# Kernel tuning notes

Measured on AMD Instinct MI355X. Metric: run time of the kernel, lower is better.

Reference implementation:

```python
import jax, jax.numpy as jnp
import numpy as np

B_, S_, F_ = 2, 1024, 1024          # batch, seq_len, in_features
H_, D_, R_ = 8, 64, 2               # num_heads, head_dim, rank
EPS_NORM = 1e-6
EPS_RMS = 1e-6


def setup_inputs() -> dict:
    key = jax.random.key(0)
    ks = jax.random.split(key, 9)
    inputs = jax.random.normal(ks[0], (B_, S_, F_), dtype=jnp.float32)
    mask = jax.random.bernoulli(ks[1], 0.05, (B_, S_))  # episode-reset mask
    carry = jax.random.normal(ks[2], (B_, H_, D_, D_), dtype=jnp.float32) * 0.05
    lecun = 1.0 / np.sqrt(F_)
    Wq = jax.random.normal(ks[3], (F_, H_ * D_), dtype=jnp.float32) * lecun
    Wk = jax.random.normal(ks[4], (F_, H_ * R_ * D_), dtype=jnp.float32) * lecun
    Wv = jax.random.normal(ks[5], (F_, H_ * R_ * D_), dtype=jnp.float32) * lecun
    Wb = jax.random.normal(ks[6], (F_, H_ * R_), dtype=jnp.float32) * lecun
    rms_scale = jnp.ones((H_ * D_,), dtype=jnp.float32)
    Wo = jax.random.normal(ks[7], (H_ * D_, F_), dtype=jnp.float32) * (1.0 / np.sqrt(H_ * D_))
    bo = jnp.zeros((F_,), dtype=jnp.float32)
    return dict(inputs=inputs, mask=mask, carry=carry, Wq=Wq, Wk=Wk, Wv=Wv,
                Wb=Wb, rms_scale=rms_scale, Wo=Wo, bo=bo)


def reference(inputs, mask, carry, Wq, Wk, Wv, Wb, rms_scale, Wo, bo):
    B, S, F = inputs.shape
    H, D, R = H_, D_, R_

    q = jax.nn.silu(inputs @ Wq).reshape(B, S, H, D)
    k = jax.nn.silu((inputs @ Wk).reshape(B, S, H, R, D))
    v = (inputs @ Wv).reshape(B, S, H, R, D)
    beta = jax.nn.sigmoid((inputs @ Wb).reshape(B, S, H, R))

    q = q / (jnp.linalg.norm(q, axis=-1, keepdims=True) + EPS_NORM)
    k = k / (jnp.linalg.norm(k, axis=-1, keepdims=True) + EPS_NORM)

    # Rank-R Householder-style per-timestep transition: loop over small fixed rank
    A = jnp.broadcast_to(jnp.eye(D, dtype=inputs.dtype), (B, S, H, D, D))
    Bst = jnp.zeros((B, S, H, D, D), dtype=inputs.dtype)
    for r in range(R):
        kr = k[:, :, :, r]          # [B,S,H,D]
        vr = v[:, :, :, r]          # [B,S,H,D]
        br = beta[:, :, :, r]       # [B,S,H]
        Ak = jnp.einsum('bshij,bshj->bshi', A, kr)
        A = A - jnp.einsum('bshi,bsh,bshj->bshij', Ak, br, kr)
        Bk = jnp.einsum('bshij,bshj->bshi', Bst, kr)
        Bst = Bst + jnp.einsum('bshi,bsh,bshj->bshij', vr - Bk, br, kr)

    # zero the transition where mask=1 (state reset)
    A = A * (1.0 - mask.astype(A.dtype))[:, :, None, None, None]

    def binary_operator(lhs, rhs):
        a_i, b_i = lhs
        a_j, b_j = rhs
        return jnp.matmul(a_i, a_j), jnp.matmul(b_i, a_j) + b_j

    A, Bst = jax.lax.associative_scan(binary_operator, (A, Bst), axis=1)

    carry_seq = jnp.matmul(carry[:, None], A) + Bst        # [B,S,H,D,D]
    x = jnp.einsum('bshij,bshj->bshi', carry_seq, q).reshape(B, S, H * D)
    x = x * jax.lax.rsqrt(jnp.mean(x * x, axis=-1, keepdims=True) + EPS_RMS) * rms_scale
    y = x @ Wo + bo
    return carry_seq[:, -1], y
```

## Files before the change

### kernel.cpp

```cpp
#include <hip/hip_runtime.h>
#include <hip/hip_bf16.h>

#define B_ 2
#define S_ 1024
#define F_ 1024
#define H_ 8
#define D_ 64
#define R_ 2
#define BH (B_*H_)
#define NC 16
#define CL (S_/NC)

#define QOFF 0
#define KOFF 512
#define VOFF 1536
#define BOFF 2560
#define NPROJ 2624

typedef __bf16 bf16x8 __attribute__((ext_vector_type(8)));
typedef unsigned short ushort8 __attribute__((ext_vector_type(8)));
typedef float f32x4 __attribute__((ext_vector_type(4)));

__device__ __forceinline__ unsigned short f2bf(float f) {
    unsigned u = __builtin_bit_cast(unsigned, f);
    unsigned r = u + 0x7FFFu + ((u >> 16) & 1u);
    return (unsigned short)(r >> 16);
}

__device__ __forceinline__ void gload_lds16(const void* g, void* l) {
    __builtin_amdgcn_global_load_lds(
        (const __attribute__((address_space(1))) void*)g,
        (__attribute__((address_space(3))) void*)l, 16, 0, 0);
}

template<int CTRL>
__device__ __forceinline__ float dppf(float x) {
    return __builtin_bit_cast(float, __builtin_amdgcn_update_dpp(
        0, __builtin_bit_cast(int, x), CTRL, 0xF, 0xF, true));
}
__device__ __forceinline__ float qsum8(float x) {
    x += dppf<0xB1>(x);
    x += dppf<0x4E>(x);
    x += dppf<0x141>(x);
    return x;
}

__global__ void k_mask_prep(const void* __restrict__ mraw, float* __restrict__ maskf, int n) {
    __shared__ int fmt;
    int t = threadIdx.x;
    if (t == 0) fmt = 0;
    __syncthreads();
    const unsigned int* u32 = (const unsigned int*)mraw;
    for (int g = t; g < n / 4; g += blockDim.x) {
        unsigned int v = u32[g];
        if (v == 0x3F800000u) atomicMax(&fmt, 2);
        else if (v != 0u && v != 1u) atomicMax(&fmt, 1);
    }
    __syncthreads();
    int f = fmt;
    const unsigned char* u8 = (const unsigned char*)mraw;
    const float* f32 = (const float*)mraw;
    for (int i = t; i < n; i += blockDim.x) {
        float mv;
        if (f == 1)      mv = u8[i] ? 1.f : 0.f;
        else if (f == 2) mv = (f32[i] != 0.f) ? 1.f : 0.f;
        else             mv = (u32[i] != 0u) ? 1.f : 0.f;
        maskf[i] = mv;
    }
}

__global__ void k_f32_to_bf16(const float* __restrict__ s, unsigned short* __restrict__ d, int n) {
    int i = (blockIdx.x * blockDim.x + threadIdx.x) * 4;
    if (i < n) {
        float4 v = *(const float4*)&s[i];
        d[i + 0] = f2bf(v.x); d[i + 1] = f2bf(v.y);
        d[i + 2] = f2bf(v.z); d[i + 3] = f2bf(v.w);
    }
}

__global__ __launch_bounds__(256) void k_transpose_to_bf16(
    const float* __restrict__ src, unsigned short* __restrict__ dst, int K, int N)
{
    __shared__ float tile[32][33];
    int bx = blockIdx.x, by = blockIdx.y;
    int tx = threadIdx.x & 31, ty = threadIdx.x >> 5;
#pragma unroll
    for (int i = 0; i < 32; i += 8)
        tile[ty + i][tx] = src[(size_t)(by * 32 + ty + i) * N + bx * 32 + tx];
    __syncthreads();
#pragma unroll
    for (int i = 0; i < 32; i += 8)
        dst[(size_t)(bx * 32 + ty + i) * K + by * 32 + tx] = f2bf(tile[tx][ty + i]);
}

__global__ void k_wb_pad(const float* __restrict__ Wb, unsigned short* __restrict__ dst) {
    int row = blockIdx.x;
    int c0 = threadIdx.x * 4;
#pragma unroll
    for (int c = c0; c < c0 + 4; ++c)
        dst[(size_t)row * 1024 + c] = (row < 16) ? f2bf(Wb[(size_t)c * 16 + row]) : (unsigned short)0;
}

__global__ __launch_bounds__(256) void k_gemm_bf16(
    const unsigned short* __restrict__ A, const unsigned short* __restrict__ Bt,
    const float* __restrict__ bias, float* __restrict__ C,
    int M, int N, int K)
{
    constexpr int BM = 128, BN = 64, BK = 64;
    __shared__ unsigned short sA[BM * BK];
    __shared__ unsigned short sB[BN * BK];
    int t = threadIdx.x;
    int w = t >> 6, l = t & 63;
    int rowb = blockIdx.y * BM, colb = blockIdx.x * BN;
    int wr = w >> 1, wc = w & 1;
    int fr = l & 15, kgrp = l >> 4;

    f32x4 acc[4][2];
#pragma unroll
    for (int m = 0; m < 4; ++m)
#pragma unroll
        for (int n = 0; n < 2; ++n) acc[m][n] = (f32x4){0.f, 0.f, 0.f, 0.f};

    int lrow_off = l >> 3;
    int kg_phys = l & 7;

    for (int k0 = 0; k0 < K; k0 += BK) {
        __syncthreads();
#pragma unroll
        for (int is = 0; is < 4; ++is) {
            int r0 = (w * 4 + is) * 8;
            int row = r0 + lrow_off;
            int kg_log = kg_phys ^ (row & 7);
            gload_lds16(A + (size_t)(rowb + row) * K + k0 + kg_log * 8, &sA[r0 * BK]);
        }
#pragma unroll
        for (int is = 0; is < 2; ++is) {
            int r0 = (w * 2 + is) * 8;
            int row = r0 + lrow_off;
            int kg_log = kg_phys ^ (row & 7);
            gload_lds16(Bt + (size_t)(colb + row) * K + k0 + kg_log * 8, &sB[r0 * BK]);
        }
        asm volatile("s_waitcnt vmcnt(0)" ::: "memory");
        __syncthreads();

#pragma unroll
        for (int kk = 0; kk < BK; kk += 32) {
            int kg = (kk >> 3) + kgrp;
            bf16x8 af[4], bfv[2];
#pragma unroll
            for (int m = 0; m < 4; ++m) {
                int row = wr * 64 + m * 16 + fr;
                ushort8 raw = *(const ushort8*)&sA[row * BK + (kg ^ (row & 7)) * 8];
                af[m] = __builtin_bit_cast(bf16x8, raw);
            }
#pragma unroll
            for (int n = 0; n < 2; ++n) {
                int row = wc * 32 + n * 16 + fr;
                ushort8 raw = *(const ushort8*)&sB[row * BK + (kg ^ (row & 7)) * 8];
                bfv[n] = __builtin_bit_cast(bf16x8, raw);
            }
#pragma unroll
            for (int m = 0; m < 4; ++m)
#pragma unroll
                for (int n = 0; n < 2; ++n)
                    acc[m][n] = __builtin_amdgcn_mfma_f32_16x16x32_bf16(af[m], bfv[n], acc[m][n], 0, 0, 0);
        }
    }

#pragma unroll
    for (int m = 0; m < 4; ++m)
#pragma unroll
        for (int n = 0; n < 2; ++n) {
            int grow0 = rowb + wr * 64 + m * 16 + kgrp * 4;
            int gcol  = colb + wc * 32 + n * 16 + fr;
            float bv = bias ? bias[gcol] : 0.f;
#pragma unroll
            for (int r = 0; r < 4; ++r)
                C[(size_t)(grow0 + r) * N + gcol] = acc[m][n][r] + bv;
        }
}

__global__ void k_silu_norm(float* __restrict__ buf, int ngroups,
                            int gshift, int gmask, int rowstride, int coloff) {
    int w = threadIdx.x >> 6;
    int l = threadIdx.x & 63;
    int g = blockIdx.x * 4 + w;
    if (g >= ngroups) return;
    size_t idx = (size_t)(g >> gshift) * rowstride + coloff + ((g & gmask) << 6) + l;
    float x = buf[idx];
    float s = x / (1.f + expf(-x));
    float ss = s * s;
#pragma unroll
    for (int m = 1; m < 64; m <<= 1) ss += __shfl_xor(ss, m);
    float nrm = sqrtf(ss) + 1e-6f;
    buf[idx] = s / nrm;
}

__global__ __launch_bounds__(1024) void k_chunk_transfer(
    const float* __restrict__ proj, const float* __restrict__ maskf,
    float* __restrict__ Ac, float* __restrict__ Bc, float* __restrict__ ab)
{
    int c = blockIdx.x;
    int bh = blockIdx.y;
    int b = bh >> 3, h = bh & 7;
    int t = threadIdx.x;
    int half = t >> 9;
    int tt = t & 511;
    int i = tt >> 3;
    int sub = tt & 7;
    int e0 = sub * 8;
    __shared__ float sK[CL][128];
    __shared__ float sQ[CL][64];
    __shared__ float4 sScal[CL];
    __shared__ float4 sDots[CL];

    size_t tokbase = (size_t)(b * S_ + c * CL);
#pragma unroll
    for (int it = 0; it < (CL * 32) / 1024; ++it) {
        int f = it * 1024 + t;
        int tok = f >> 5, wi = f & 31;
        *(float4*)&sK[tok][wi * 4] = *(const float4*)&proj[(tokbase + tok) * NPROJ + KOFF + h * 128 + wi * 4];
    }
    {
        int f = t;
        int tok = f >> 4, wi = f & 15;
        *(float4*)&sQ[tok][wi * 4] = *(const float4*)&proj[(tokbase + tok) * NPROJ + QOFF + h * 64 + wi * 4];
    }
    if (t < CL) {
        float r0 = proj[(tokbase + t) * NPROJ + BOFF + h * 2 + 0];
        float r1 = proj[(tokbase + t) * NPROJ + BOFF + h * 2 + 1];
        float ms = 1.f - maskf[tokbase + t];
        sScal[t] = make_float4(1.f / (1.f + expf(-r0)), 1.f / (1.f + expf(-r1)), ms, 0.f);
    }
    __syncthreads();

    if (t < 512) {
        int tok = t >> 3, s8 = (t & 7) * 8;
        float p01 = 0.f, p0q = 0.f, p1q = 0.f;
#pragma unroll
        for (int e = 0; e < 8; ++e) {
            float k0e = sK[tok][s8 + e];
            float k1e = sK[tok][64 + s8 + e];
            float qe  = sQ[tok][s8 + e];
            p01 = fmaf(k0e, k1e, p01);
            p0q = fmaf(k0e, qe,  p0q);
            p1q = fmaf(k1e, qe,  p1q);
        }
        p01 = qsum8(p01); p0q = qsum8(p0q); p1q = qsum8(p1q);
        if ((t & 7) == 0) sDots[tok] = make_float4(p01, p0q, p1q, 0.f);
    }
    __syncthreads();

    float St[8];
#pragma unroll
    for (int j = 0; j < 8; ++j)
        St[j] = (half == 0 && e0 + j == i) ? 1.f : 0.f;

    const float* vbase = &proj[tokbase * NPROJ + VOFF + h * 128];
    float v0 = 0.f, v1 = 0.f;
    if (half) { v0 = vbase[i]; v1 = vbase[64 + i]; }

    float* abdst = ab + ((size_t)bh * NC + c) * (size_t)(CL * 128) + half * 64 + i;

    for (int sl = 0; sl < CL; ++sl) {
        float vc0 = v0, vc1 = v1;
        if (half && sl + 1 < CL) {
            const float* nb = vbase + (size_t)(sl + 1) * NPROJ;
            v0 = nb[i]; v1 = nb[64 + i];
        }
        float4 sc = sScal[sl];
        float4 dt = sDots[sl];
        if (sc.z == 0.f) {
#pragma unroll
            for (int j = 0; j < 8; ++j) St[j] = 0.f;
        }
        float k0[8], k1[8], qq[8];
        *(float4*)&k0[0] = *(const float4*)&sK[sl][e0];
        *(float4*)&k0[4] = *(const float4*)&sK[sl][e0 + 4];
        *(float4*)&k1[0] = *(const float4*)&sK[sl][64 + e0];
        *(float4*)&k1[4] = *(const float4*)&sK[sl][64 + e0 + 4];
        *(float4*)&qq[0] = *(const float4*)&sQ[sl][e0];
        *(float4*)&qq[4] = *(const float4*)&sQ[sl][e0 + 4];
        float a0 = 0.f, a1 = 0.f, b0 = 0.f, b1 = 0.f, c0v = 0.f, c1v = 0.f;
#pragma unroll
        for (int q = 0; q < 4; ++q) {
            a0 = fmaf(St[q],     k0[q],     a0);
            a1 = fmaf(St[4 + q], k0[4 + q], a1);
            b0 = fmaf(St[q],     k1[q],     b0);
            b1 = fmaf(St[4 + q], k1[4 + q], b1);
            c0v = fmaf(St[q],     qq[q],     c0v);
            c1v = fmaf(St[4 + q], qq[4 + q], c1v);
        }
        float d0 = qsum8(a0 + a1);
        float d1 = qsum8(b0 + b1);
        float dq = qsum8(c0v + c1v);
        float c0, c1;
        if (half == 0) {
            c0 = -sc.x * d0;
            float u1 = fmaf(c0, dt.x, d1);
            c1 = -sc.y * u1;
        } else {
            c0 = sc.x * (vc0 - d0);
            float u1 = fmaf(c0, dt.x, d1);
            c1 = sc.y * (vc1 - u1);
        }
        float xv = fmaf(c1, dt.z, fmaf(c0, dt.y, dq));
        if (sub == 0) abdst[sl * 128] = xv;
#pragma unroll
        for (int j = 0; j < 8; ++j) {
            St[j] = fmaf(c0, k0[j], St[j]);
            St[j] = fmaf(c1, k1[j], St[j]);
        }
    }
    float* dst = (half == 0 ? Ac : Bc) + ((size_t)bh * NC + c) * 4096 + (size_t)i * 64 + e0;
    *(float4*)&dst[0] = make_float4(St[0], St[1], St[2], St[3]);
    *(float4*)&dst[4] = make_float4(St[4], St[5], St[6], St[7]);
}

__global__ __launch_bounds__(256) void k_combine(
    const float* __restrict__ Ac, const float* __restrict__ Bc,
    const float* __restrict__ carry, float* __restrict__ S0,
    float* __restrict__ carry_out)
{
    constexpr int SP = 68;
    int blk = blockIdx.x;
    int bh = blk >> 2, rg = blk & 3;
    int t = threadIdx.x;
    int i = t >> 4;
    int j0 = (t & 15) * 4;
    int gi = rg * 16 + i;
    __shared__ float sA[2][64 * 64];
    __shared__ float sS[16 * SP];

    size_t cb0 = (size_t)bh * NC * 4096;
#pragma unroll
    for (int s = 0; s < 4; ++s)
        gload_lds16(Ac + cb0 + (size_t)(s * 256 + t) * 4, &sA[0][(size_t)(s * 256 + (t & 192)) * 4]);
    float4 rB = *(const float4*)&Bc[cb0 + (size_t)gi * 64 + j0];
    float4 racc = *(const float4*)&carry[(size_t)bh * 4096 + (size_t)gi * 64 + j0];
    *(float4*)&sS[i * SP + j0] = racc;
    asm volatile("s_waitcnt vmcnt(0)" ::: "memory");
    __syncthreads();

    for (int c = 0; c < NC; ++c) {
        int cur = c & 1;
        size_t cb = cb0 + (size_t)c * 4096;
        float4 rBn;
        if (c + 1 < NC) {
#pragma unroll
            for (int s = 0; s < 4; ++s)
                gload_lds16(Ac + cb + 4096 + (size_t)(s * 256 + t) * 4,
                            &sA[cur ^ 1][(size_t)(s * 256 + (t & 192)) * 4]);
            rBn = *(const float4*)&Bc[cb + 4096 + (size_t)gi * 64 + j0];
        }
        *(float4*)&S0[cb + (size_t)gi * 64 + j0] = racc;
        float4 acc = rB;
        float4 ac2 = make_float4(0.f, 0.f, 0.f, 0.f);
#pragma unroll
        for (int p4 = 0; p4 < 16; p4 += 2) {
            float4 s0v = *(const float4*)&sS[i * SP + p4 * 4];
            float4 s1v = *(const float4*)&sS[i * SP + p4 * 4 + 4];
            float4 a0 = *(const float4*)&sA[cur][(p4 * 4 + 0) * 64 + j0];
            float4 a1 = *(const float4*)&sA[cur][(p4 * 4 + 1) * 64 + j0];
            float4 a2 = *(const float4*)&sA[cur][(p4 * 4 + 2) * 64 + j0];
            float4 a3 = *(const float4*)&sA[cur][(p4 * 4 + 3) * 64 + j0];
            float4 a4 = *(const float4*)&sA[cur][(p4 * 4 + 4) * 64 + j0];
            float4 a5 = *(const float4*)&sA[cur][(p4 * 4 + 5) * 64 + j0];
            float4 a6 = *(const float4*)&sA[cur][(p4 * 4 + 6) * 64 + j0];
            float4 a7 = *(const float4*)&sA[cur][(p4 * 4 + 7) * 64 + j0];
            acc.x = fmaf(s0v.x, a0.x, acc.x); acc.y = fmaf(s0v.x, a0.y, acc.y);
            acc.z = fmaf(s0v.x, a0.z, acc.z); acc.w = fmaf(s0v.x, a0.w, acc.w);
            ac2.x = fmaf(s0v.y, a1.x, ac2.x); ac2.y = fmaf(s0v.y, a1.y, ac2.y);
            ac2.z = fmaf(s0v.y, a1.z, ac2.z); ac2.w = fmaf(s0v.y, a1.w, ac2.w);
            acc.x = fmaf(s0v.z, a2.x, acc.x); acc.y = fmaf(s0v.z, a2.y, acc.y);
            acc.z = fmaf(s0v.z, a2.z, acc.z); acc.w = fmaf(s0v.z, a2.w, acc.w);
            ac2.x = fmaf(s0v.w, a3.x, ac2.x); ac2.y = fmaf(s0v.w, a3.y, ac2.y);
            ac2.z = fmaf(s0v.w, a3.z, ac2.z); ac2.w = fmaf(s0v.w, a3.w, ac2.w);
            acc.x = fmaf(s1v.x, a4.x, acc.x); acc.y = fmaf(s1v.x, a4.y, acc.y);
            acc.z = fmaf(s1v.x, a4.z, acc.z); acc.w = fmaf(s1v.x, a4.w, acc.w);
            ac2.x = fmaf(s1v.y, a5.x, ac2.x); ac2.y = fmaf(s1v.y, a5.y, ac2.y);
            ac2.z = fmaf(s1v.y, a5.z, ac2.z); ac2.w = fmaf(s1v.y, a5.w, ac2.w);
            acc.x = fmaf(s1v.z, a6.x, acc.x); acc.y = fmaf(s1v.z, a6.y, acc.y);
            acc.z = fmaf(s1v.z, a6.z, acc.z); acc.w = fmaf(s1v.z, a6.w, acc.w);
            ac2.x = fmaf(s1v.w, a7.x, ac2.x); ac2.y = fmaf(s1v.w, a7.y, ac2.y);
            ac2.z = fmaf(s1v.w, a7.z, ac2.z); ac2.w = fmaf(s1v.w, a7.w, ac2.w);
        }
        acc.x += ac2.x; acc.y += ac2.y; acc.z += ac2.z; acc.w += ac2.w;
        __syncthreads();
        *(float4*)&sS[i * SP + j0] = acc;
        racc = acc;
        rB = rBn;
        asm volatile("s_waitcnt vmcnt(0)" ::: "memory");
        __syncthreads();
    }
    *(float4*)&carry_out[(size_t)bh * 4096 + (size_t)gi * 64 + j0] = racc;
}

__global__ __launch_bounds__(256) void k_xgemm(
    const float* __restrict__ ab, const float* __restrict__ S0,
    float* __restrict__ proj)
{
    constexpr int P = 67;
    int c = blockIdx.x, bh = blockIdx.y;
    int b = bh >> 3, h = bh & 7;
    int t = threadIdx.x;
    __shared__ float sAaT[64 * P];
    __shared__ float sS0T[64 * P];
    size_t abbase = ((size_t)bh * NC + c) * (size_t)(CL * 128);
    size_t s0base = ((size_t)bh * NC + c) * 4096;

#pragma unroll
    for (int it = 0; it < 4; ++it) {
        int f = it * 256 + t;
        int r = f >> 4, p0 = (f & 15) * 4;
        float4 va = *(const float4*)&ab[abbase + (size_t)r * 128 + p0];
        sAaT[(p0 + 0) * P + r] = va.x; sAaT[(p0 + 1) * P + r] = va.y;
        sAaT[(p0 + 2) * P + r] = va.z; sAaT[(p0 + 3) * P + r] = va.w;
        float4 vs = *(const float4*)&S0[s0base + (size_t)r * 64 + p0];
        sS0T[(p0 + 0) * P + r] = vs.x; sS0T[(p0 + 1) * P + r] = vs.y;
        sS0T[(p0 + 2) * P + r] = vs.z; sS0T[(p0 + 3) * P + r] = vs.w;
    }
    __syncthreads();

    int s0r = (t >> 4) * 4;
    int i0 = (t & 15) * 4;
    size_t tokbase = (size_t)(b * S_ + c * CL);
    float4 acc[4];
#pragma unroll
    for (int a = 0; a < 4; ++a)
        acc[a] = *(const float4*)&ab[abbase + (size_t)(s0r + a) * 128 + 64 + i0];
#pragma unroll 8
    for (int p = 0; p < 64; ++p) {
        float4 aa = *(const float4*)&sAaT[p * P + s0r];
        float4 ss = *(const float4*)&sS0T[p * P + i0];
        acc[0].x = fmaf(aa.x, ss.x, acc[0].x); acc[0].y = fmaf(aa.x, ss.y, acc[0].y);
        acc[0].z = fmaf(aa.x, ss.z, acc[0].z); acc[0].w = fmaf(aa.x, ss.w, acc[0].w);
        acc[1].x = fmaf(aa.y, ss.x, acc[1].x); acc[1].y = fmaf(aa.y, ss.y, acc[1].y);
        acc[1].z = fmaf(aa.y, ss.z, acc[1].z); acc[1].w = fmaf(aa.y, ss.w, acc[1].w);
        acc[2].x = fmaf(aa.z, ss.x, acc[2].x); acc[2].y = fmaf(aa.z, ss.y, acc[2].y);
        acc[2].z = fmaf(aa.z, ss.z, acc[2].z); acc[2].w = fmaf(aa.z, ss.w, acc[2].w);
        acc[3].x = fmaf(aa.w, ss.x, acc[3].x); acc[3].y = fmaf(aa.w, ss.y, acc[3].y);
        acc[3].z = fmaf(aa.w, ss.z, acc[3].z); acc[3].w = fmaf(aa.w, ss.w, acc[3].w);
    }
#pragma unroll
    for (int a = 0; a < 4; ++a)
        *(float4*)&proj[(tokbase + s0r + a) * NPROJ + QOFF + h * 64 + i0] = acc[a];
}

__global__ void k_rms_bf16(const float* __restrict__ proj, const float* __restrict__ scale,
                           unsigned short* __restrict__ xo) {
    int w = threadIdx.x >> 6;
    int l = threadIdx.x & 63;
    size_t row = (size_t)blockIdx.x * 4 + w;
    float4 v0 = *(const float4*)&proj[row * NPROJ + l * 8];
    float4 v1 = *(const float4*)&proj[row * NPROJ + l * 8 + 4];
    float ss = v0.x * v0.x + v0.y * v0.y + v0.z * v0.z + v0.w * v0.w
             + v1.x * v1.x + v1.y * v1.y + v1.z * v1.z + v1.w * v1.w;
#pragma unroll
    for (int m = 1; m < 64; m <<= 1) ss += __shfl_xor(ss, m);
    float sc = rsqrtf(ss * (1.f / 512.f) + 1e-6f);
    float4 s0 = *(const float4*)&scale[l * 8];
    float4 s1 = *(const float4*)&scale[l * 8 + 4];
    ushort8 o;
    o[0] = f2bf(v0.x * sc * s0.x); o[1] = f2bf(v0.y * sc * s0.y);
    o[2] = f2bf(v0.z * sc * s0.z); o[3] = f2bf(v0.w * sc * s0.w);
    o[4] = f2bf(v1.x * sc * s1.x); o[5] = f2bf(v1.y * sc * s1.y);
    o[6] = f2bf(v1.z * sc * s1.z); o[7] = f2bf(v1.w * sc * s1.w);
    *(ushort8*)&xo[row * 512 + l * 8] = o;
}

extern "C" void kernel_launch(void* const* d_in, const int* in_sizes, int n_in,
                              void* d_out, int out_size, void* d_ws, size_t ws_size,
                              hipStream_t stream) {
    const float* inputs    = (const float*)d_in[0];
    const void*  mask      = d_in[1];
    const float* carry     = (const float*)d_in[2];
    const float* Wq        = (const float*)d_in[3];
    const float* Wk        = (const float*)d_in[4];
    const float* Wv        = (const float*)d_in[5];
    const float* Wb        = (const float*)d_in[6];
    const float* rms_scale = (const float*)d_in[7];
    const float* Wo        = (const float*)d_in[8];
    const float* bo        = (const float*)d_in[9];

    float* out_carry = (float*)d_out;
    float* out_y     = (float*)d_out + (size_t)B_ * H_ * D_ * D_;

    const int M = B_ * S_;
    float* ws = (float*)d_ws;
    size_t o = 0;
    float* proj = ws + o; o += (size_t)M * NPROJ;
    float* mf   = ws + o; o += (size_t)M;
    float* Ac   = ws + o; o += (size_t)BH * NC * 4096;
    float* Bc   = ws + o; o += (size_t)BH * NC * 4096;
    float* S0   = ws + o; o += (size_t)BH * NC * 4096;
    float* abuf = ws + o; o += (size_t)BH * NC * CL * 128;
    unsigned short* wt = (unsigned short*)(ws + o); o += (size_t)NPROJ * 512;
    unsigned short* inb = (unsigned short*)Bc;
    unsigned short* xbf = (unsigned short*)Ac;

    k_mask_prep<<<1, 256, 0, stream>>>(mask, mf, M);
    k_f32_to_bf16<<<(M * 1024) / 1024, 256, 0, stream>>>(inputs, inb, M * 1024);

    k_transpose_to_bf16<<<dim3(512 / 32, 1024 / 32), 256, 0, stream>>>(Wq, wt + (size_t)QOFF * 1024, 1024, 512);
    k_transpose_to_bf16<<<dim3(1024 / 32, 1024 / 32), 256, 0, stream>>>(Wk, wt + (size_t)KOFF * 1024, 1024, 1024);
    k_transpose_to_bf16<<<dim3(1024 / 32, 1024 / 32), 256, 0, stream>>>(Wv, wt + (size_t)VOFF * 1024, 1024, 1024);
    k_wb_pad<<<64, 256, 0, stream>>>(Wb, wt + (size_t)BOFF * 1024);

    k_gemm_bf16<<<dim3(NPROJ / 64, M / 128), 256, 0, stream>>>(inb, wt, nullptr, proj, M, NPROJ, 1024);

    k_silu_norm<<<(M * 8) / 4, 256, 0, stream>>>(proj, M * 8, 3, 7, NPROJ, QOFF);
    k_silu_norm<<<(M * 16) / 4, 256, 0, stream>>>(proj, M * 16, 4, 15, NPROJ, KOFF);

    k_chunk_transfer<<<dim3(NC, BH), 1024, 0, stream>>>(proj, mf, Ac, Bc, abuf);
    k_combine<<<BH * 4, 256, 0, stream>>>(Ac, Bc, carry, S0, out_carry);
    k_xgemm<<<dim3(NC, BH), 256, 0, stream>>>(abuf, S0, proj);

    k_rms_bf16<<<M / 4, 256, 0, stream>>>(proj, rms_scale, xbf);

    k_transpose_to_bf16<<<dim3(1024 / 32, 512 / 32), 256, 0, stream>>>(Wo, wt, 512, 1024);
    k_gemm_bf16<<<dim3(1024 / 64, M / 128), 256, 0, stream>>>(xbf, wt, bo, out_y, M, 1024, 512);
}
```

Measured before the change: 138.5 us.

## Split scan into 32 short chunks with pairwise merge and fixup

The sequential per-chunk transfer kernel now processes 32 chunks of 32 tokens instead of 16 chunks of 64. This halves the serial loop length per block and doubles the block count. Adjacent chunk pairs are merged into 16 transitions for the existing inter-chunk combine. A new fixup kernel then recovers the start state of each even sub-chunk from the combined state. The change adds two small 64x64 matmul kernel launches and extra workspace traffic in exchange for a shorter serial critical path in the chunk scan.

```diff
diff --git a/kernel.cpp b/kernel.cpp
--- a/kernel.cpp
+++ b/kernel.cpp
@@ -9,7 +9,8 @@
 #define R_ 2
 #define BH (B_*H_)
 #define NC 16
-#define CL (S_/NC)
+#define NCT 32
+#define CT (S_/NCT)
 
 #define QOFF 0
 #define KOFF 512
@@ -209,24 +210,21 @@
     int i = tt >> 3;
     int sub = tt & 7;
     int e0 = sub * 8;
-    __shared__ float sK[CL][128];
-    __shared__ float sQ[CL][64];
-    __shared__ float4 sScal[CL];
-    __shared__ float4 sDots[CL];
-
-    size_t tokbase = (size_t)(b * S_ + c * CL);
-#pragma unroll
-    for (int it = 0; it < (CL * 32) / 1024; ++it) {
-        int f = it * 1024 + t;
-        int tok = f >> 5, wi = f & 31;
+    __shared__ float sK[CT][128];
+    __shared__ float sQ[CT][64];
+    __shared__ float4 sScal[CT];
+    __shared__ float4 sDots[CT];
+
+    size_t tokbase = (size_t)(b * S_ + c * CT);
+    {
+        int tok = t >> 5, wi = t & 31;
         *(float4*)&sK[tok][wi * 4] = *(const float4*)&proj[(tokbase + tok) * NPROJ + KOFF + h * 128 + wi * 4];
     }
-    {
-        int f = t;
-        int tok = f >> 4, wi = f & 15;
+    if (t < CT * 16) {
+        int tok = t >> 4, wi = t & 15;
         *(float4*)&sQ[tok][wi * 4] = *(const float4*)&proj[(tokbase + tok) * NPROJ + QOFF + h * 64 + wi * 4];
     }
-    if (t < CL) {
+    if (t < CT) {
         float r0 = proj[(tokbase + t) * NPROJ + BOFF + h * 2 + 0];
         float r1 = proj[(tokbase + t) * NPROJ + BOFF + h * 2 + 1];
         float ms = 1.f - maskf[tokbase + t];
@@ -234,7 +232,7 @@
     }
     __syncthreads();
 
-    if (t < 512) {
+    if (t < CT * 8) {
         int tok = t >> 3, s8 = (t & 7) * 8;
         float p01 = 0.f, p0q = 0.f, p1q = 0.f;
 #pragma unroll
@@ -260,11 +258,11 @@
     float v0 = 0.f, v1 = 0.f;
     if (half) { v0 = vbase[i]; v1 = vbase[64 + i]; }
 
-    float* abdst = ab + ((size_t)bh * NC + c) * (size_t)(CL * 128) + half * 64 + i;
-
-    for (int sl = 0; sl < CL; ++sl) {
+    float* abdst = ab + ((size_t)bh * NCT + c) * (size_t)(CT * 128) + half * 64 + i;
+
+    for (int sl = 0; sl < CT; ++sl) {
         float vc0 = v0, vc1 = v1;
-        if (half && sl + 1 < CL) {
+        if (half && sl + 1 < CT) {
             const float* nb = vbase + (size_t)(sl + 1) * NPROJ;
             v0 = nb[i]; v1 = nb[64 + i];
         }
@@ -312,14 +310,72 @@
             St[j] = fmaf(c1, k1[j], St[j]);
         }
     }
-    float* dst = (half == 0 ? Ac : Bc) + ((size_t)bh * NC + c) * 4096 + (size_t)i * 64 + e0;
+    float* dst = (half == 0 ? Ac : Bc) + ((size_t)bh * NCT + c) * 4096 + (size_t)i * 64 + e0;
     *(float4*)&dst[0] = make_float4(St[0], St[1], St[2], St[3]);
     *(float4*)&dst[4] = make_float4(St[4], St[5], St[6], St[7]);
 }
 
+__device__ __forceinline__ void stage_padded(const float* __restrict__ g, float* lds, int t) {
+#pragma unroll
+    for (int s = 0; s < 4; ++s) {
+        int f = s * 256 + t;
+        float4 v = *(const float4*)&g[(size_t)f * 4];
+        int r = f >> 4, c = (f & 15) * 4;
+        *(float4*)&lds[r * 68 + c] = v;
+    }
+}
+
+__global__ __launch_bounds__(256) void k_merge(
+    const float* __restrict__ Ac32, const float* __restrict__ Bc32,
+    float* __restrict__ Ac16, float* __restrict__ Bc16)
+{
+    int g = blockIdx.x, bh = blockIdx.y;
+    size_t li = ((size_t)bh * NCT + 2 * g) * 4096;
+    size_t ri = li + 4096;
+    int t = threadIdx.x;
+    int i = t >> 2, j0 = (t & 3) * 16;
+    __shared__ float sAl[64 * 68];
+    __shared__ float sBl[64 * 68];
+    __shared__ float sAr[4096];
+
+#pragma unroll
+    for (int s = 0; s < 4; ++s)
+        gload_lds16(Ac32 + ri + (size_t)(s * 256 + t) * 4, &sAr[(size_t)(s * 256 + (t & 192)) * 4]);
+    stage_padded(Ac32 + li, sAl, t);
+    stage_padded(Bc32 + li, sBl, t);
+    float4 aB[4], aA[4];
+#pragma unroll
+    for (int q = 0; q < 4; ++q) {
+        aB[q] = *(const float4*)&Bc32[ri + (size_t)i * 64 + j0 + q * 4];
+        aA[q] = make_float4(0.f, 0.f, 0.f, 0.f);
+    }
+    asm volatile("s_waitcnt vmcnt(0)" ::: "memory");
+    __syncthreads();
+
+#pragma unroll 4
+    for (int pp = 0; pp < 64; ++pp) {
+        float la = sAl[i * 68 + pp];
+        float lb = sBl[i * 68 + pp];
+#pragma unroll
+        for (int q = 0; q < 4; ++q) {
+            float4 ar = *(const float4*)&sAr[pp * 64 + j0 + q * 4];
+            aA[q].x = fmaf(la, ar.x, aA[q].x); aA[q].y = fmaf(la, ar.y, aA[q].y);
+            aA[q].z = fmaf(la, ar.z, aA[q].z); aA[q].w = fmaf(la, ar.w, aA[q].w);
+            aB[q].x = fmaf(lb, ar.x, aB[q].x); aB[q].y = fmaf(lb, ar.y, aB[q].y);
+            aB[q].z = fmaf(lb, ar.z, aB[q].z); aB[q].w = fmaf(lb, ar.w, aB[q].w);
+        }
+    }
+    size_t od = ((size_t)bh * NC + g) * 4096 + (size_t)i * 64 + j0;
+#pragma unroll
+    for (int q = 0; q < 4; ++q) {
+        *(float4*)&Ac16[od + q * 4] = aA[q];
+        *(float4*)&Bc16[od + q * 4] = aB[q];
+    }
+}
+
 __global__ __launch_bounds__(256) void k_combine(
     const float* __restrict__ Ac, const float* __restrict__ Bc,
-    const float* __restrict__ carry, float* __restrict__ S0,
+    const float* __restrict__ carry, float* __restrict__ S0ac,
     float* __restrict__ carry_out)
 {
     constexpr int SP = 68;
@@ -353,7 +409,7 @@
                             &sA[cur ^ 1][(size_t)(s * 256 + (t & 192)) * 4]);
             rBn = *(const float4*)&Bc[cb + 4096 + (size_t)gi * 64 + j0];
         }
-        *(float4*)&S0[cb + (size_t)gi * 64 + j0] = racc;
+        *(float4*)&S0ac[((size_t)bh * NCT + 2 * c + 1) * 4096 + (size_t)gi * 64 + j0] = racc;
         float4 acc = rB;
         float4 ac2 = make_float4(0.f, 0.f, 0.f, 0.f);
 #pragma unroll
@@ -396,54 +452,92 @@
     *(float4*)&carry_out[(size_t)bh * 4096 + (size_t)gi * 64 + j0] = racc;
 }
 
+__global__ __launch_bounds__(256) void k_fixup(
+    float* __restrict__ Ac32, const float* __restrict__ Bc32)
+{
+    int g = blockIdx.x, bh = blockIdx.y;
+    int t = threadIdx.x;
+    int i = t >> 2, j0 = (t & 3) * 16;
+    size_t sEven = ((size_t)bh * NCT + 2 * g) * 4096;
+    size_t sOdd  = sEven + 4096;
+    __shared__ float sS[64 * 68];
+    __shared__ float sA[4096];
+
+#pragma unroll
+    for (int s = 0; s < 4; ++s)
+        gload_lds16(Ac32 + sEven + (size_t)(s * 256 + t) * 4, &sA[(size_t)(s * 256 + (t & 192)) * 4]);
+    stage_padded(Ac32 + sOdd, sS, t);
+    float4 acc[4];
+#pragma unroll
+    for (int q = 0; q < 4; ++q)
+        acc[q] = *(const float4*)&Bc32[sEven + (size_t)i * 64 + j0 + q * 4];
+    asm volatile("s_waitcnt vmcnt(0)" ::: "memory");
+    __syncthreads();
+
+#pragma unroll 4
+    for (int pp = 0; pp < 64; ++pp) {
+        float s = sS[i * 68 + pp];
+#pragma unroll
+        for (int q = 0; q < 4; ++q) {
+            float4 ar = *(const float4*)&sA[pp * 64 + j0 + q * 4];
+            acc[q].x = fmaf(s, ar.x, acc[q].x); acc[q].y = fmaf(s, ar.y, acc[q].y);
+            acc[q].z = fmaf(s, ar.z, acc[q].z); acc[q].w = fmaf(s, ar.w, acc[q].w);
+        }
+    }
+#pragma unroll
+    for (int q = 0; q < 4; ++q)
+        *(float4*)&Ac32[sEven + (size_t)i * 64 + j0 + q * 4] = acc[q];
+}
+
 __global__ __launch_bounds__(256) void k_xgemm(
-    const float* __restrict__ ab, const float* __restrict__ S0,
+    const float* __restrict__ ab, const float* __restrict__ S0ac,
     float* __restrict__ proj)
 {
-    constexpr int P = 67;
     int c = blockIdx.x, bh = blockIdx.y;
     int b = bh >> 3, h = bh & 7;
     int t = threadIdx.x;
-    __shared__ float sAaT[64 * P];
-    __shared__ float sS0T[64 * P];
-    size_t abbase = ((size_t)bh * NC + c) * (size_t)(CL * 128);
-    size_t s0base = ((size_t)bh * NC + c) * 4096;
-
+    __shared__ float sAaT[64 * 33];
+    __shared__ float sS0T[64 * 67];
+    size_t abbase = ((size_t)bh * NCT + c) * (size_t)(CT * 128);
+    size_t s0base = ((size_t)bh * NCT + (c ^ 1)) * 4096;
+
+#pragma unroll
+    for (int it = 0; it < 2; ++it) {
+        int f = it * 256 + t;
+        int r = f >> 4, p0 = (f & 15) * 4;
+        float4 va = *(const float4*)&ab[abbase + (size_t)r * 128 + p0];
+        sAaT[(p0 + 0) * 33 + r] = va.x; sAaT[(p0 + 1) * 33 + r] = va.y;
+        sAaT[(p0 + 2) * 33 + r] = va.z; sAaT[(p0 + 3) * 33 + r] = va.w;
+    }
 #pragma unroll
     for (int it = 0; it < 4; ++it) {
         int f = it * 256 + t;
         int r = f >> 4, p0 = (f & 15) * 4;
-        float4 va = *(const float4*)&ab[abbase + (size_t)r * 128 + p0];
-        sAaT[(p0 + 0) * P + r] = va.x; sAaT[(p0 + 1) * P + r] = va.y;
-        sAaT[(p0 + 2) * P + r] = va.z; sAaT[(p0 + 3) * P + r] = va.w;
-        float4 vs = *(const float4*)&S0[s0base + (size_t)r * 64 + p0];
-        sS0T[(p0 + 0) * P + r] = vs.x; sS0T[(p0 + 1) * P + r] = vs.y;
-        sS0T[(p0 + 2) * P + r] = vs.z; sS0T[(p0 + 3) * P + r] = vs.w;
-    }
-    __syncthreads();
-
-    int s0r = (t >> 4) * 4;
+        float4 vs = *(const float4*)&S0ac[s0base + (size_t)r * 64 + p0];
+        sS0T[(p0 + 0) * 67 + r] = vs.x; sS0T[(p0 + 1) * 67 + r] = vs.y;
+        sS0T[(p0 + 2) * 67 + r] = vs.z; sS0T[(p0 + 3) * 67 + r] = vs.w;
+    }
+    __syncthreads();
+
+    int s0r = (t >> 4) * 2;
     int i0 = (t & 15) * 4;
-    size_t tokbase = (size_t)(b * S_ + c * CL);
-    float4 acc[4];
-#pragma unroll
-    for (int a = 0; a < 4; ++a)
+    size_t tokbase = (size_t)(b * S_ + c * CT);
+    float4 acc[2];
+#pragma unroll
+    for (int a = 0; a < 2; ++a)
         acc[a] = *(const float4*)&ab[abbase + (size_t)(s0r + a) * 128 + 64 + i0];
 #pragma unroll 8
     for (int p = 0; p < 64; ++p) {
-        float4 aa = *(const float4*)&sAaT[p * P + s0r];
-        float4 ss = *(const float4*)&sS0T[p * P + i0];
-        acc[0].x = fmaf(aa.x, ss.x, acc[0].x); acc[0].y = fmaf(aa.x, ss.y, acc[0].y);
-        acc[0].z = fmaf(aa.x, ss.z, acc[0].z); acc[0].w = fmaf(aa.x, ss.w, acc[0].w);
-        acc[1].x = fmaf(aa.y, ss.x, acc[1].x); acc[1].y = fmaf(aa.y, ss.y, acc[1].y);
-        acc[1].z = fmaf(aa.y, ss.z, acc[1].z); acc[1].w = fmaf(aa.y, ss.w, acc[1].w);
-        acc[2].x = fmaf(aa.z, ss.x, acc[2].x); acc[2].y = fmaf(aa.z, ss.y, acc[2].y);
-        acc[2].z = fmaf(aa.z, ss.z, acc[2].z); acc[2].w = fmaf(aa.z, ss.w, acc[2].w);
-        acc[3].x = fmaf(aa.w, ss.x, acc[3].x); acc[3].y = fmaf(aa.w, ss.y, acc[3].y);
-        acc[3].z = fmaf(aa.w, ss.z, acc[3].z); acc[3].w = fmaf(aa.w, ss.w, acc[3].w);
-    }
-#pragma unroll
-    for (int a = 0; a < 4; ++a)
+        float aa0 = sAaT[p * 33 + s0r];
+        float aa1 = sAaT[p * 33 + s0r + 1];
+        float4 ss = *(const float4*)&sS0T[p * 67 + i0];
+        acc[0].x = fmaf(aa0, ss.x, acc[0].x); acc[0].y = fmaf(aa0, ss.y, acc[0].y);
+        acc[0].z = fmaf(aa0, ss.z, acc[0].z); acc[0].w = fmaf(aa0, ss.w, acc[0].w);
+        acc[1].x = fmaf(aa1, ss.x, acc[1].x); acc[1].y = fmaf(aa1, ss.y, acc[1].y);
+        acc[1].z = fmaf(aa1, ss.z, acc[1].z); acc[1].w = fmaf(aa1, ss.w, acc[1].w);
+    }
+#pragma unroll
+    for (int a = 0; a < 2; ++a)
         *(float4*)&proj[(tokbase + s0r + a) * NPROJ + QOFF + h * 64 + i0] = acc[a];
 }
 
@@ -489,15 +583,16 @@
     const int M = B_ * S_;
     float* ws = (float*)d_ws;
     size_t o = 0;
-    float* proj = ws + o; o += (size_t)M * NPROJ;
-    float* mf   = ws + o; o += (size_t)M;
-    float* Ac   = ws + o; o += (size_t)BH * NC * 4096;
-    float* Bc   = ws + o; o += (size_t)BH * NC * 4096;
-    float* S0   = ws + o; o += (size_t)BH * NC * 4096;
-    float* abuf = ws + o; o += (size_t)BH * NC * CL * 128;
+    float* proj  = ws + o; o += (size_t)M * NPROJ;
+    float* mf    = ws + o; o += (size_t)M;
+    float* Ac32  = ws + o; o += (size_t)BH * NCT * 4096;
+    float* Bc32  = ws + o; o += (size_t)BH * NCT * 4096;
+    float* Ac16  = ws + o; o += (size_t)BH * NC * 4096;
+    float* Bc16  = ws + o; o += (size_t)BH * NC * 4096;
+    float* abuf  = ws + o; o += (size_t)BH * NCT * CT * 128;
     unsigned short* wt = (unsigned short*)(ws + o); o += (size_t)NPROJ * 512;
-    unsigned short* inb = (unsigned short*)Bc;
-    unsigned short* xbf = (unsigned short*)Ac;
+    unsigned short* inb = (unsigned short*)Bc32;
+    unsigned short* xbf = (unsigned short*)Ac16;
 
     k_mask_prep<<<1, 256, 0, stream>>>(mask, mf, M);
     k_f32_to_bf16<<<(M * 1024) / 1024, 256, 0, stream>>>(inputs, inb, M * 1024);
@@ -512,9 +607,11 @@
     k_silu_norm<<<(M * 8) / 4, 256, 0, stream>>>(proj, M * 8, 3, 7, NPROJ, QOFF);
     k_silu_norm<<<(M * 16) / 4, 256, 0, stream>>>(proj, M * 16, 4, 15, NPROJ, KOFF);
 
-    k_chunk_transfer<<<dim3(NC, BH), 1024, 0, stream>>>(proj, mf, Ac, Bc, abuf);
-    k_combine<<<BH * 4, 256, 0, stream>>>(Ac, Bc, carry, S0, out_carry);
-    k_xgemm<<<dim3(NC, BH), 256, 0, stream>>>(abuf, S0, proj);
+    k_chunk_transfer<<<dim3(NCT, BH), 1024, 0, stream>>>(proj, mf, Ac32, Bc32, abuf);
+    k_merge<<<dim3(NC, BH), 256, 0, stream>>>(Ac32, Bc32, Ac16, Bc16);
+    k_combine<<<BH * 4, 256, 0, stream>>>(Ac16, Bc16, carry, Ac32, out_carry);
+    k_fixup<<<dim3(NC, BH), 256, 0, stream>>>(Ac32, Bc32);
+    k_xgemm<<<dim3(NCT, BH), 256, 0, stream>>>(abuf, Ac32, proj);
 
     k_rms_bf16<<<M / 4, 256, 0, stream>>>(proj, rms_scale, xbf);
 
```

Result: slower. 154.1 us (+11.3%).
